# Kernel optimization log

Hardware: AMD Instinct MI355X
Metric: run time of the kernel (lower is better)

## Reference

```python
import jax, jax.numpy as jnp
import numpy as np

N, E, D, C, H = 50000, 800000, 128, 64, 2
NEG_SLOPE = 0.2


def gat_layer(x, src, dst, W, a_src, a_dst, b, heads, concat):
    # PyG GATConv (eval mode: attention dropout disabled), add_self_loops already in src/dst.
    n = x.shape[0]
    c = W.shape[1] // heads
    xl = (x @ W).reshape(n, heads, c)                      # [N,H,C]
    s = jnp.einsum('nhc,hc->nh', xl, a_src)                # alpha_src per node
    d = jnp.einsum('nhc,hc->nh', xl, a_dst)                # alpha_dst per node
    e = jax.nn.leaky_relu(s[src] + d[dst], NEG_SLOPE)      # [E,H]
    emax = jax.lax.stop_gradient(jax.ops.segment_max(e, dst, num_segments=n))
    ex = jnp.exp(e - emax[dst])
    denom = jax.ops.segment_sum(ex, dst, num_segments=n)   # every node has a self-loop -> denom > 0
    alpha = ex / denom[dst]                                # softmax over incoming edges
    msg = xl[src] * alpha[:, :, None]                      # [E,H,C]
    out = jax.ops.segment_sum(msg, dst, num_segments=n)    # [N,H,C]
    out = out.reshape(n, heads * c) if concat else out.mean(axis=1)
    return out + b


def setup_inputs() -> dict:
    key = jax.random.key(0)
    ks = jax.random.split(key, 16)
    x = jax.random.normal(ks[0], (N, D), dtype=jnp.float32)
    edge_index = jax.random.randint(ks[1], (2, E), 0, N, dtype=jnp.int64)
    def glorot(k, shape):
        fan = shape[0] + shape[-1]
        return jax.random.normal(k, shape, dtype=jnp.float32) * np.sqrt(2.0 / fan).astype(np.float32)
    # layer 0: D -> H*C (concat)
    W0 = glorot(ks[2], (D, H * C)); att_src0 = glorot(ks[3], (H, C)); att_dst0 = glorot(ks[4], (H, C)); b0 = jnp.zeros((H * C,), jnp.float32)
    # layer 1: H*C -> H*C (concat)
    W1 = glorot(ks[5], (H * C, H * C)); att_src1 = glorot(ks[6], (H, C)); att_dst1 = glorot(ks[7], (H, C)); b1 = jnp.zeros((H * C,), jnp.float32)
    # layer 2: H*C -> C (heads=1, concat=False)
    W2 = glorot(ks[8], (H * C, C)); att_src2 = glorot(ks[9], (1, C)); att_dst2 = glorot(ks[10], (1, C)); b2 = jnp.zeros((C,), jnp.float32)
    return dict(x=x, edge_index=edge_index,
                W0=W0, att_src0=att_src0, att_dst0=att_dst0, b0=b0,
                W1=W1, att_src1=att_src1, att_dst1=att_dst1, b1=b1,
                W2=W2, att_src2=att_src2, att_dst2=att_dst2, b2=b2)


def reference(x, edge_index, W0, att_src0, att_dst0, b0, W1, att_src1, att_dst1, b1, W2, att_src2, att_dst2, b2):
    n = x.shape[0]
    loops = jnp.arange(n, dtype=edge_index.dtype)
    src = jnp.concatenate([edge_index[0], loops])
    dst = jnp.concatenate([edge_index[1], loops])
    h = gat_layer(x, src, dst, W0, att_src0, att_dst0, b0, H, True)
    h = jax.nn.elu(h)
    h = gat_layer(h, src, dst, W1, att_src1, att_dst1, b1, H, True)
    h = jax.nn.elu(h)
    h = gat_layer(h, src, dst, W2, att_src2, att_dst2, b2, 1, False)
    return h
```

## Files before the change

### kernel.cpp

```cpp
#include <hip/hip_runtime.h>
#include <hip/hip_fp16.h>
#include <math.h>

#define NEG_SLOPE 0.2f
#define RSTRIDE_LOG 6
#define RSTRIDE (1 << RSTRIDE_LOG)

__device__ __forceinline__ float lrelu(float v) { return v > 0.0f ? v : NEG_SLOPE * v; }

typedef _Float16 half8 __attribute__((ext_vector_type(8)));
typedef float floatx4 __attribute__((ext_vector_type(4)));


__global__ __launch_bounds__(256) void cvt_wt3_init_k(const float* __restrict__ W0,
                                                      const float* __restrict__ W1,
                                                      const float* __restrict__ W2,
                                                      __half* __restrict__ Wt0,
                                                      __half* __restrict__ Wt1,
                                                      __half* __restrict__ Wt2,
                                                      int* __restrict__ cursor, int n) {
  const int i = blockIdx.x * 256 + threadIdx.x;
  const int stride = gridDim.x * 256;
  for (int k = i; k < n; k += stride) cursor[k] = k << RSTRIDE_LOG;
  if (i < 128 * 128) {
    int col = i >> 7, k = i & 127;
    Wt0[i] = __float2half(W0[k * 128 + col]);
    Wt1[i] = __float2half(W1[k * 128 + col]);
    if (col < 64) Wt2[(size_t)col * 128 + k] = __float2half(W2[k * 64 + col]);
  }
}


__global__ __launch_bounds__(256) void scatter_win_k(const int* __restrict__ src,
                                                     const int* __restrict__ dst,
                                                     int* __restrict__ cursor,
                                                     int* __restrict__ csr,
                                                     int e, int winSize) {
  const int win = blockIdx.x & 7;
  const int lo = win * winSize;
  const int hi = lo + winSize;
  const int base = (blockIdx.x >> 3) * 4096 + threadIdx.x;
  for (int t = 0; t < 16; ++t) {
    int i = base + t * 256;
    if (i < e) {
      int d = dst[i];
      if (d >= lo && d < hi) {
        int pos = atomicAdd(&cursor[d], 1);
        if (pos < ((d + 1) << RSTRIDE_LOG)) csr[pos] = src[i];
      }
    }
  }
}


template<int M, int H_, bool IN_F32>
__global__ __launch_bounds__(256) void gemm_attn_mfma_k(const void* __restrict__ Xin,
                                                        const __half* __restrict__ Wt,
                                                        const float* __restrict__ a_src,
                                                        const float* __restrict__ a_dst,
                                                        __half* __restrict__ Yh,
                                                        float* __restrict__ sArr,
                                                        float* __restrict__ dArr, int n) {
  constexpr int CT = M / 16;
  constexpr int LP = 136;
  __shared__ _Float16 Xs[64 * LP];
  __shared__ _Float16 Ws[M * LP];
  const int tid = threadIdx.x;
  const int w = tid >> 6;
  const int lane = tid & 63;
  const int l15 = lane & 15;
  const int quad = lane >> 4;
  const int rb = blockIdx.x * 64;

  if (IN_F32) {
    const float* Xf = (const float*)Xin;
    for (int t = 0; t < 8; ++t) {
      int idx = tid + t * 256;
      int r = idx >> 5, c4 = idx & 31;
      float4 v = make_float4(0.f, 0.f, 0.f, 0.f);
      if (rb + r < n) v = *(const float4*)(Xf + (size_t)(rb + r) * 128 + c4 * 4);
      __half2 a = __floats2half2_rn(v.x, v.y);
      __half2 b = __floats2half2_rn(v.z, v.w);
      uint2 pk;
      pk.x = *(unsigned int*)&a;
      pk.y = *(unsigned int*)&b;
      *(uint2*)&Xs[r * LP + c4 * 4] = pk;
    }
  } else {
    const __half* Xh = (const __half*)Xin;
    for (int t = 0; t < 4; ++t) {
      int idx = tid + t * 256;
      int r = idx >> 4, c8 = idx & 15;
      uint4 v = make_uint4(0, 0, 0, 0);
      if (rb + r < n) v = *(const uint4*)(Xh + (size_t)(rb + r) * 128 + c8 * 8);
      *(uint4*)&Xs[r * LP + c8 * 8] = v;
    }
  }
  for (int t = 0; t < CT; ++t) {
    int idx = tid + t * 256;
    int r = idx >> 4, c8 = idx & 15;
    *(uint4*)&Ws[r * LP + c8 * 8] = *(const uint4*)(Wt + (size_t)r * 128 + c8 * 8);
  }
  __syncthreads();

  floatx4 acc[CT];
  for (int c = 0; c < CT; ++c)
    for (int j = 0; j < 4; ++j) acc[c][j] = 0.f;

  const int arow = w * 16 + l15;
  for (int kq = 0; kq < 4; ++kq) {
    half8 a = *(const half8*)&Xs[arow * LP + kq * 32 + quad * 8];
    for (int c = 0; c < CT; ++c) {
      half8 b = *(const half8*)&Ws[(c * 16 + l15) * LP + kq * 32 + quad * 8];
      acc[c] = __builtin_amdgcn_mfma_f32_16x16x32_f16(a, b, acc[c], 0, 0, 0);
    }
  }

  float as[CT], ad[CT];
  for (int c = 0; c < CT; ++c) {
    as[c] = a_src[c * 16 + l15];
    ad[c] = a_dst[c * 16 + l15];
  }

  for (int c = 0; c < CT; ++c) {
    for (int r = 0; r < 4; ++r) {
      int row = rb + w * 16 + quad * 4 + r;
      if (row < n) Yh[(size_t)row * M + c * 16 + l15] = __float2half(acc[c][r]);
    }
  }

  for (int r = 0; r < 4; ++r) {
    int row = rb + w * 16 + quad * 4 + r;
    float s0 = 0.f, d0 = 0.f, s1 = 0.f, d1 = 0.f;
    if (H_ == 2) {
      for (int c = 0; c < CT / 2; ++c) {
        s0 += acc[c][r] * as[c];
        d0 += acc[c][r] * ad[c];
      }
      for (int c = CT / 2; c < CT; ++c) {
        s1 += acc[c][r] * as[c];
        d1 += acc[c][r] * ad[c];
      }
    } else {
      for (int c = 0; c < CT; ++c) {
        s0 += acc[c][r] * as[c];
        d0 += acc[c][r] * ad[c];
      }
    }
    for (int o = 1; o < 16; o <<= 1) {
      s0 += __shfl_xor(s0, o);
      d0 += __shfl_xor(d0, o);
      if (H_ == 2) {
        s1 += __shfl_xor(s1, o);
        d1 += __shfl_xor(d1, o);
      }
    }
    if (l15 == 0 && row < n) {
      if (H_ == 2) {
        sArr[row * 2] = s0;
        sArr[row * 2 + 1] = s1;
        dArr[row * 2] = d0;
        dArr[row * 2 + 1] = d1;
      } else {
        sArr[row] = s0;
        dArr[row] = d0;
      }
    }
  }
}


__global__ __launch_bounds__(256) void edge2h_k(const __half* __restrict__ xlh,
                                                const float* __restrict__ sArr,
                                                const float* __restrict__ dArr,
                                                const float* __restrict__ bias,
                                                const int* __restrict__ cursor,
                                                const int* __restrict__ csr,
                                                __half* __restrict__ outh, int n) {
  const int tid = threadIdx.x;
  const int wid = tid >> 6;
  const int lane = tid & 63;
  const int sub = lane >> 4;
  const int l16 = lane & 15;
  const int nodeBase = blockIdx.x * 16;

  __shared__ int curS[16];
  __shared__ int idxS[16 * RSTRIDE];
  if (tid < 16) {
    int nn = nodeBase + tid;
    curS[tid] = (nn < n) ? cursor[nn] : 0;
  }
  __syncthreads();
  for (int t = tid; t < 16 * RSTRIDE; t += 256) {
    int li2 = t >> RSTRIDE_LOG, j = t & (RSTRIDE - 1);
    int node2 = nodeBase + li2;
    if (node2 < n) {
      int dg = curS[li2] - (node2 << RSTRIDE_LOG);
      if (j < dg) idxS[t] = csr[(node2 << RSTRIDE_LOG) + j];
    }
  }
  __syncthreads();

  const int li = (wid << 2) + sub;
  const int node = nodeBase + li;
  if (node >= n) return;
  int deg = curS[li] - (node << RSTRIDE_LOG);
  if (deg > RSTRIDE) deg = RSTRIDE;
  const int head = l16 >> 3;
  const uint4* __restrict__ xq = (const uint4*)xlh;
  const float dnsel = dArr[node * 2 + head];

  float svS = sArr[node * 2 + head];
  uint4 pS = xq[(size_t)node * 16 + l16];

  float a0 = 0.f, a1 = 0.f, a2 = 0.f, a3 = 0.f;
  float a4 = 0.f, a5 = 0.f, a6 = 0.f, a7 = 0.f;
  float den = 0.f;

  const int* __restrict__ ip = &idxS[li << RSTRIDE_LOG];
  int j = 0;
  for (; j + 4 <= deg; j += 4) {
    int idx[4];
    float sv[4];
    uint4 p[4];
#pragma unroll
    for (int t = 0; t < 4; ++t) idx[t] = ip[j + t];
#pragma unroll
    for (int t = 0; t < 4; ++t) sv[t] = sArr[idx[t] * 2 + head];
#pragma unroll
    for (int t = 0; t < 4; ++t) p[t] = xq[(size_t)idx[t] * 16 + l16];
#pragma unroll
    for (int t = 0; t < 4; ++t) {
      float w = __expf(lrelu(sv[t] + dnsel));
      den += w;
      float2 v0 = __half22float2(*(__half2*)&p[t].x);
      float2 v1 = __half22float2(*(__half2*)&p[t].y);
      float2 v2 = __half22float2(*(__half2*)&p[t].z);
      float2 v3 = __half22float2(*(__half2*)&p[t].w);
      a0 += w * v0.x; a1 += w * v0.y; a2 += w * v1.x; a3 += w * v1.y;
      a4 += w * v2.x; a5 += w * v2.y; a6 += w * v3.x; a7 += w * v3.y;
    }
  }
  for (; j < deg; ++j) {
    int i0 = ip[j];
    float sv = sArr[i0 * 2 + head];
    uint4 p = xq[(size_t)i0 * 16 + l16];
    float w = __expf(lrelu(sv + dnsel));
    den += w;
    float2 v0 = __half22float2(*(__half2*)&p.x);
    float2 v1 = __half22float2(*(__half2*)&p.y);
    float2 v2 = __half22float2(*(__half2*)&p.z);
    float2 v3 = __half22float2(*(__half2*)&p.w);
    a0 += w * v0.x; a1 += w * v0.y; a2 += w * v1.x; a3 += w * v1.y;
    a4 += w * v2.x; a5 += w * v2.y; a6 += w * v3.x; a7 += w * v3.y;
  }

  float wS = __expf(lrelu(svS + dnsel));
  den += wS;
  {
    float2 v0 = __half22float2(*(__half2*)&pS.x);
    float2 v1 = __half22float2(*(__half2*)&pS.y);
    float2 v2 = __half22float2(*(__half2*)&pS.z);
    float2 v3 = __half22float2(*(__half2*)&pS.w);
    a0 += wS * v0.x; a1 += wS * v0.y; a2 += wS * v1.x; a3 += wS * v1.y;
    a4 += wS * v2.x; a5 += wS * v2.y; a6 += wS * v3.x; a7 += wS * v3.y;
  }

  float wi = 1.f / den;
  float4 bbA = ((const float4*)bias)[l16 * 2];
  float4 bbB = ((const float4*)bias)[l16 * 2 + 1];
  float r0 = a0 * wi + bbA.x;
  float r1 = a1 * wi + bbA.y;
  float r2 = a2 * wi + bbA.z;
  float r3 = a3 * wi + bbA.w;
  float r4 = a4 * wi + bbB.x;
  float r5 = a5 * wi + bbB.y;
  float r6 = a6 * wi + bbB.z;
  float r7 = a7 * wi + bbB.w;
  r0 = r0 > 0.f ? r0 : expm1f(r0);
  r1 = r1 > 0.f ? r1 : expm1f(r1);
  r2 = r2 > 0.f ? r2 : expm1f(r2);
  r3 = r3 > 0.f ? r3 : expm1f(r3);
  r4 = r4 > 0.f ? r4 : expm1f(r4);
  r5 = r5 > 0.f ? r5 : expm1f(r5);
  r6 = r6 > 0.f ? r6 : expm1f(r6);
  r7 = r7 > 0.f ? r7 : expm1f(r7);
  __half2 h0 = __floats2half2_rn(r0, r1);
  __half2 h1 = __floats2half2_rn(r2, r3);
  __half2 h2 = __floats2half2_rn(r4, r5);
  __half2 h3 = __floats2half2_rn(r6, r7);
  uint4 pk;
  pk.x = *(unsigned int*)&h0;
  pk.y = *(unsigned int*)&h1;
  pk.z = *(unsigned int*)&h2;
  pk.w = *(unsigned int*)&h3;
  ((uint4*)outh)[(size_t)node * 16 + l16] = pk;
}

__global__ __launch_bounds__(256) void edge1h_k(const __half* __restrict__ xlh,
                                                const float* __restrict__ sArr,
                                                const float* __restrict__ dArr,
                                                const float* __restrict__ bias,
                                                const int* __restrict__ cursor,
                                                const int* __restrict__ csr,
                                                float* __restrict__ outp, int n) {
  const int tid = threadIdx.x;
  const int wid = tid >> 6;
  const int lane = tid & 63;
  const int sub = lane >> 4;
  const int l16 = lane & 15;
  const int nodeBase = blockIdx.x * 16;

  __shared__ int curS[16];
  __shared__ int idxS[16 * RSTRIDE];
  if (tid < 16) {
    int nn = nodeBase + tid;
    curS[tid] = (nn < n) ? cursor[nn] : 0;
  }
  __syncthreads();
  for (int t = tid; t < 16 * RSTRIDE; t += 256) {
    int li2 = t >> RSTRIDE_LOG, j = t & (RSTRIDE - 1);
    int node2 = nodeBase + li2;
    if (node2 < n) {
      int dg = curS[li2] - (node2 << RSTRIDE_LOG);
      if (j < dg) idxS[t] = csr[(node2 << RSTRIDE_LOG) + j];
    }
  }
  __syncthreads();

  const int li = (wid << 2) + sub;
  const int node = nodeBase + li;
  if (node >= n) return;
  int deg = curS[li] - (node << RSTRIDE_LOG);
  if (deg > RSTRIDE) deg = RSTRIDE;
  const uint2* __restrict__ xq = (const uint2*)xlh;
  const float dn = dArr[node];

  float svS = sArr[node];
  uint2 pS = xq[(size_t)node * 16 + l16];

  float a0 = 0.f, a1 = 0.f, a2 = 0.f, a3 = 0.f;
  float den = 0.f;

  const int* __restrict__ ip = &idxS[li << RSTRIDE_LOG];
  int j = 0;
  for (; j + 4 <= deg; j += 4) {
    int idx[4];
    float sv[4];
    uint2 p[4];
#pragma unroll
    for (int t = 0; t < 4; ++t) idx[t] = ip[j + t];
#pragma unroll
    for (int t = 0; t < 4; ++t) sv[t] = sArr[idx[t]];
#pragma unroll
    for (int t = 0; t < 4; ++t) p[t] = xq[(size_t)idx[t] * 16 + l16];
#pragma unroll
    for (int t = 0; t < 4; ++t) {
      float w = __expf(lrelu(sv[t] + dn));
      den += w;
      float2 v0 = __half22float2(*(__half2*)&p[t].x);
      float2 v1 = __half22float2(*(__half2*)&p[t].y);
      a0 += w * v0.x; a1 += w * v0.y; a2 += w * v1.x; a3 += w * v1.y;
    }
  }
  for (; j < deg; ++j) {
    int i0 = ip[j];
    float sv = sArr[i0];
    uint2 p = xq[(size_t)i0 * 16 + l16];
    float w = __expf(lrelu(sv + dn));
    den += w;
    float2 v0 = __half22float2(*(__half2*)&p.x);
    float2 v1 = __half22float2(*(__half2*)&p.y);
    a0 += w * v0.x; a1 += w * v0.y; a2 += w * v1.x; a3 += w * v1.y;
  }

  float wS = __expf(lrelu(svS + dn));
  den += wS;
  {
    float2 v0 = __half22float2(*(__half2*)&pS.x);
    float2 v1 = __half22float2(*(__half2*)&pS.y);
    a0 += wS * v0.x; a1 += wS * v0.y; a2 += wS * v1.x; a3 += wS * v1.y;
  }

  float wi = 1.f / den;
  float4 bb = ((const float4*)bias)[l16];
  float4 r;
  r.x = a0 * wi + bb.x;
  r.y = a1 * wi + bb.y;
  r.z = a2 * wi + bb.z;
  r.w = a3 * wi + bb.w;
  ((float4*)outp)[(size_t)node * 16 + l16] = r;
}


extern "C" void kernel_launch(void* const* d_in, const int* in_sizes, int n_in,
                              void* d_out, int out_size, void* d_ws, size_t ws_size,
                              hipStream_t stream) {
  const float* x  = (const float*)d_in[0];
  const int* ei   = (const int*)d_in[1];
  const float* W0 = (const float*)d_in[2];
  const float* as0 = (const float*)d_in[3];
  const float* ad0 = (const float*)d_in[4];
  const float* b0 = (const float*)d_in[5];
  const float* W1 = (const float*)d_in[6];
  const float* as1 = (const float*)d_in[7];
  const float* ad1 = (const float*)d_in[8];
  const float* b1 = (const float*)d_in[9];
  const float* W2 = (const float*)d_in[10];
  const float* as2 = (const float*)d_in[11];
  const float* ad2 = (const float*)d_in[12];
  const float* b2 = (const float*)d_in[13];
  float* out = (float*)d_out;

  const int n = in_sizes[0] / 128;
  const int e = in_sizes[1] / 2;
  const int* srcIdx = ei;
  const int* dstIdx = ei + e;

  float* ws = (float*)d_ws;
  float* sArr = ws;
  float* dArr = sArr + (size_t)n * 2;
  __half* xlh = (__half*)(dArr + (size_t)n * 2);
  __half* bufHh = xlh + (size_t)n * 128;
  __half* Wt0 = bufHh + (size_t)n * 128;
  __half* Wt1 = Wt0 + 128 * 128;
  __half* Wt2 = Wt1 + 128 * 128;
  int* csr = (int*)(Wt2 + 64 * 128);
  int* cursor = csr + (size_t)n * RSTRIDE;

  const int nb = (n + 255) / 256;
  const int winSize = (n + 7) / 8;
  const int gwin = 8 * ((e + 4095) / 4096);

  cvt_wt3_init_k<<<nb, 256, 0, stream>>>(W0, W1, W2, Wt0, Wt1, Wt2, cursor, n);
  scatter_win_k<<<gwin, 256, 0, stream>>>(srcIdx, dstIdx, cursor, csr, e, winSize);

  const int gb = (n + 63) / 64;
  const int gq = (n + 15) / 16;

  gemm_attn_mfma_k<128, 2, true><<<gb, 256, 0, stream>>>(x, Wt0, as0, ad0, xlh, sArr, dArr, n);
  edge2h_k<<<gq, 256, 0, stream>>>(xlh, sArr, dArr, b0, cursor, csr, bufHh, n);

  gemm_attn_mfma_k<128, 2, false><<<gb, 256, 0, stream>>>(bufHh, Wt1, as1, ad1, xlh, sArr, dArr, n);
  edge2h_k<<<gq, 256, 0, stream>>>(xlh, sArr, dArr, b1, cursor, csr, bufHh, n);

  gemm_attn_mfma_k<64, 1, false><<<gb, 256, 0, stream>>>(bufHh, Wt2, as2, ad2, xlh, sArr, dArr, n);
  edge1h_k<<<gq, 256, 0, stream>>>(xlh, sArr, dArr, b2, cursor, csr, out, n);
}
```

Measured before the change: 260.4 us.

## Fuse CSR scatter into first GEMM launch to overlap independent work

```diff
diff --git a/kernel.cpp b/kernel.cpp
--- a/kernel.cpp
+++ b/kernel.cpp
@@ -31,46 +31,23 @@
 }
 
 
-__global__ __launch_bounds__(256) void scatter_win_k(const int* __restrict__ src,
-                                                     const int* __restrict__ dst,
-                                                     int* __restrict__ cursor,
-                                                     int* __restrict__ csr,
-                                                     int e, int winSize) {
-  const int win = blockIdx.x & 7;
-  const int lo = win * winSize;
-  const int hi = lo + winSize;
-  const int base = (blockIdx.x >> 3) * 4096 + threadIdx.x;
-  for (int t = 0; t < 16; ++t) {
-    int i = base + t * 256;
-    if (i < e) {
-      int d = dst[i];
-      if (d >= lo && d < hi) {
-        int pos = atomicAdd(&cursor[d], 1);
-        if (pos < ((d + 1) << RSTRIDE_LOG)) csr[pos] = src[i];
-      }
-    }
-  }
-}
-
-
 template<int M, int H_, bool IN_F32>
-__global__ __launch_bounds__(256) void gemm_attn_mfma_k(const void* __restrict__ Xin,
-                                                        const __half* __restrict__ Wt,
-                                                        const float* __restrict__ a_src,
-                                                        const float* __restrict__ a_dst,
-                                                        __half* __restrict__ Yh,
-                                                        float* __restrict__ sArr,
-                                                        float* __restrict__ dArr, int n) {
+__device__ __forceinline__ void gemm_body(_Float16* Xs, _Float16* Ws,
+                                          const void* __restrict__ Xin,
+                                          const __half* __restrict__ Wt,
+                                          const float* __restrict__ a_src,
+                                          const float* __restrict__ a_dst,
+                                          __half* __restrict__ Yh,
+                                          float* __restrict__ sArr,
+                                          float* __restrict__ dArr, int n, int tile) {
   constexpr int CT = M / 16;
   constexpr int LP = 136;
-  __shared__ _Float16 Xs[64 * LP];
-  __shared__ _Float16 Ws[M * LP];
   const int tid = threadIdx.x;
   const int w = tid >> 6;
   const int lane = tid & 63;
   const int l15 = lane & 15;
   const int quad = lane >> 4;
-  const int rb = blockIdx.x * 64;
+  const int rb = tile * 64;
 
   if (IN_F32) {
     const float* Xf = (const float*)Xin;
@@ -164,6 +141,56 @@
       } else {
         sArr[row] = s0;
         dArr[row] = d0;
+      }
+    }
+  }
+}
+
+
+template<int M, int H_, bool IN_F32>
+__global__ __launch_bounds__(256) void gemm_attn_mfma_k(const void* __restrict__ Xin,
+                                                        const __half* __restrict__ Wt,
+                                                        const float* __restrict__ a_src,
+                                                        const float* __restrict__ a_dst,
+                                                        __half* __restrict__ Yh,
+                                                        float* __restrict__ sArr,
+                                                        float* __restrict__ dArr, int n) {
+  __shared__ _Float16 Xs[64 * 136];
+  __shared__ _Float16 Ws[M * 136];
+  gemm_body<M, H_, IN_F32>(Xs, Ws, Xin, Wt, a_src, a_dst, Yh, sArr, dArr, n, blockIdx.x);
+}
+
+
+__global__ __launch_bounds__(256) void gemm0_scatter_k(const void* __restrict__ Xin,
+                                                       const __half* __restrict__ Wt0,
+                                                       const float* __restrict__ a_src,
+                                                       const float* __restrict__ a_dst,
+                                                       __half* __restrict__ Yh,
+                                                       float* __restrict__ sArr,
+                                                       float* __restrict__ dArr, int n, int gb,
+                                                       const int* __restrict__ src,
+                                                       const int* __restrict__ dst,
+                                                       int* __restrict__ cursor,
+                                                       int* __restrict__ csr,
+                                                       int e, int winSize) {
+  __shared__ _Float16 Xs[64 * 136];
+  __shared__ _Float16 Ws[128 * 136];
+  if ((int)blockIdx.x < gb) {
+    gemm_body<128, 2, true>(Xs, Ws, Xin, Wt0, a_src, a_dst, Yh, sArr, dArr, n, blockIdx.x);
+  } else {
+    const int vb = blockIdx.x - gb;
+    const int win = vb & 7;
+    const int lo = win * winSize;
+    const int hi = lo + winSize;
+    const int base = (vb >> 3) * 4096 + threadIdx.x;
+    for (int t = 0; t < 16; ++t) {
+      int i = base + t * 256;
+      if (i < e) {
+        int d = dst[i];
+        if (d >= lo && d < hi) {
+          int pos = atomicAdd(&cursor[d], 1);
+          if (pos < ((d + 1) << RSTRIDE_LOG)) csr[pos] = src[i];
+        }
       }
     }
   }
@@ -431,14 +458,13 @@
   const int nb = (n + 255) / 256;
   const int winSize = (n + 7) / 8;
   const int gwin = 8 * ((e + 4095) / 4096);
-
-  cvt_wt3_init_k<<<nb, 256, 0, stream>>>(W0, W1, W2, Wt0, Wt1, Wt2, cursor, n);
-  scatter_win_k<<<gwin, 256, 0, stream>>>(srcIdx, dstIdx, cursor, csr, e, winSize);
-
   const int gb = (n + 63) / 64;
   const int gq = (n + 15) / 16;
 
-  gemm_attn_mfma_k<128, 2, true><<<gb, 256, 0, stream>>>(x, Wt0, as0, ad0, xlh, sArr, dArr, n);
+  cvt_wt3_init_k<<<nb, 256, 0, stream>>>(W0, W1, W2, Wt0, Wt1, Wt2, cursor, n);
+
+  gemm0_scatter_k<<<gb + gwin, 256, 0, stream>>>(x, Wt0, as0, ad0, xlh, sArr, dArr, n, gb,
+                                                 srcIdx, dstIdx, cursor, csr, e, winSize);
   edge2h_k<<<gq, 256, 0, stream>>>(xlh, sArr, dArr, b0, cursor, csr, bufHh, n);
 
   gemm_attn_mfma_k<128, 2, false><<<gb, 256, 0, stream>>>(bufHh, Wt1, as1, ad1, xlh, sArr, dArr, n);
```

Result: no change. 265.5 us (+2.0%).

## Merge CSR scatter into layer-0 GEMM launch as extra blocks

Applied to the files above, without the earlier changes.

```diff
diff --git a/kernel.cpp b/kernel.cpp
--- a/kernel.cpp
+++ b/kernel.cpp
@@ -31,23 +31,111 @@
 }
 
 
-__global__ __launch_bounds__(256) void scatter_win_k(const int* __restrict__ src,
-                                                     const int* __restrict__ dst,
-                                                     int* __restrict__ cursor,
-                                                     int* __restrict__ csr,
-                                                     int e, int winSize) {
-  const int win = blockIdx.x & 7;
-  const int lo = win * winSize;
-  const int hi = lo + winSize;
-  const int base = (blockIdx.x >> 3) * 4096 + threadIdx.x;
-  for (int t = 0; t < 16; ++t) {
-    int i = base + t * 256;
-    if (i < e) {
-      int d = dst[i];
-      if (d >= lo && d < hi) {
-        int pos = atomicAdd(&cursor[d], 1);
-        if (pos < ((d + 1) << RSTRIDE_LOG)) csr[pos] = src[i];
+__global__ __launch_bounds__(256) void gemm0_scatter_k(const float* __restrict__ Xf,
+                                                       const __half* __restrict__ Wt,
+                                                       const float* __restrict__ a_src,
+                                                       const float* __restrict__ a_dst,
+                                                       __half* __restrict__ Yh,
+                                                       float* __restrict__ sArr,
+                                                       float* __restrict__ dArr, int n, int gb,
+                                                       const int* __restrict__ src,
+                                                       const int* __restrict__ dst,
+                                                       int* __restrict__ cursor,
+                                                       int* __restrict__ csr,
+                                                       int e, int winSize) {
+  constexpr int CT = 8;
+  constexpr int LP = 136;
+  __shared__ _Float16 Xs[64 * LP];
+  const int tid = threadIdx.x;
+
+  if ((int)blockIdx.x >= gb) {
+    const int vb = blockIdx.x - gb;
+    const int win = vb & 7;
+    const int lo = win * winSize;
+    const int hi = lo + winSize;
+    const int base = (vb >> 3) * 4096 + tid;
+    for (int t = 0; t < 16; ++t) {
+      int i = base + t * 256;
+      if (i < e) {
+        int d = dst[i];
+        if (d >= lo && d < hi) {
+          int pos = atomicAdd(&cursor[d], 1);
+          if (pos < ((d + 1) << RSTRIDE_LOG)) csr[pos] = src[i];
+        }
       }
+    }
+    return;
+  }
+
+  const int w = tid >> 6;
+  const int lane = tid & 63;
+  const int l15 = lane & 15;
+  const int quad = lane >> 4;
+  const int rb = blockIdx.x * 64;
+
+  for (int t = 0; t < 8; ++t) {
+    int idx = tid + t * 256;
+    int r = idx >> 5, c4 = idx & 31;
+    float4 v = make_float4(0.f, 0.f, 0.f, 0.f);
+    if (rb + r < n) v = *(const float4*)(Xf + (size_t)(rb + r) * 128 + c4 * 4);
+    __half2 a = __floats2half2_rn(v.x, v.y);
+    __half2 b = __floats2half2_rn(v.z, v.w);
+    uint2 pk;
+    pk.x = *(unsigned int*)&a;
+    pk.y = *(unsigned int*)&b;
+    *(uint2*)&Xs[r * LP + c4 * 4] = pk;
+  }
+  __syncthreads();
+
+  floatx4 acc[CT];
+  for (int c = 0; c < CT; ++c)
+    for (int j = 0; j < 4; ++j) acc[c][j] = 0.f;
+
+  const int arow = w * 16 + l15;
+  const _Float16* __restrict__ Wg = (const _Float16*)Wt;
+  for (int kq = 0; kq < 4; ++kq) {
+    half8 a = *(const half8*)&Xs[arow * LP + kq * 32 + quad * 8];
+    for (int c = 0; c < CT; ++c) {
+      half8 b = *(const half8*)&Wg[(size_t)(c * 16 + l15) * 128 + kq * 32 + quad * 8];
+      acc[c] = __builtin_amdgcn_mfma_f32_16x16x32_f16(a, b, acc[c], 0, 0, 0);
+    }
+  }
+
+  float as[CT], ad[CT];
+  for (int c = 0; c < CT; ++c) {
+    as[c] = a_src[c * 16 + l15];
+    ad[c] = a_dst[c * 16 + l15];
+  }
+
+  for (int c = 0; c < CT; ++c) {
+    for (int r = 0; r < 4; ++r) {
+      int row = rb + w * 16 + quad * 4 + r;
+      if (row < n) Yh[(size_t)row * 128 + c * 16 + l15] = __float2half(acc[c][r]);
+    }
+  }
+
+  for (int r = 0; r < 4; ++r) {
+    int row = rb + w * 16 + quad * 4 + r;
+    float s0 = 0.f, d0 = 0.f, s1 = 0.f, d1 = 0.f;
+    for (int c = 0; c < CT / 2; ++c) {
+      s0 += acc[c][r] * as[c];
+      d0 += acc[c][r] * ad[c];
+    }
+    for (int c = CT / 2; c < CT; ++c) {
+      s1 += acc[c][r] * as[c];
+      d1 += acc[c][r] * ad[c];
+    }
+    for (int o = 1; o < 16; o <<= 1) {
+      s0 += __shfl_xor(s0, o);
+      d0 += __shfl_xor(d0, o);
+      s1 += __shfl_xor(s1, o);
+      d1 += __shfl_xor(d1, o);
+    }
+    if (l15 == 0 && row < n) {
+      sArr[row * 2] = s0;
+      sArr[row * 2 + 1] = s1;
+      dArr[row * 2] = d0;
+      dArr[row * 2 + 1] = d1;
     }
   }
 }
@@ -431,14 +519,13 @@
   const int nb = (n + 255) / 256;
   const int winSize = (n + 7) / 8;
   const int gwin = 8 * ((e + 4095) / 4096);
-
-  cvt_wt3_init_k<<<nb, 256, 0, stream>>>(W0, W1, W2, Wt0, Wt1, Wt2, cursor, n);
-  scatter_win_k<<<gwin, 256, 0, stream>>>(srcIdx, dstIdx, cursor, csr, e, winSize);
-
   const int gb = (n + 63) / 64;
   const int gq = (n + 15) / 16;
 
-  gemm_attn_mfma_k<128, 2, true><<<gb, 256, 0, stream>>>(x, Wt0, as0, ad0, xlh, sArr, dArr, n);
+  cvt_wt3_init_k<<<nb, 256, 0, stream>>>(W0, W1, W2, Wt0, Wt1, Wt2, cursor, n);
+
+  gemm0_scatter_k<<<gb + gwin, 256, 0, stream>>>(x, Wt0, as0, ad0, xlh, sArr, dArr, n, gb,
+                                                 srcIdx, dstIdx, cursor, csr, e, winSize);
   edge2h_k<<<gq, 256, 0, stream>>>(xlh, sArr, dArr, b0, cursor, csr, bufHh, n);
 
   gemm_attn_mfma_k<128, 2, false><<<gb, 256, 0, stream>>>(bufHh, Wt1, as1, ad1, xlh, sArr, dArr, n);
```

Measured after the change: 265.9 us. 2.1% more time.

## Split each node's edges across four 16-lane subgroups per wavefront

Applied to the files above, without the earlier changes.

```diff
diff --git a/kernel.cpp b/kernel.cpp
--- a/kernel.cpp
+++ b/kernel.cpp
@@ -182,69 +182,39 @@
   const int lane = tid & 63;
   const int sub = lane >> 4;
   const int l16 = lane & 15;
-  const int nodeBase = blockIdx.x * 16;
-
-  __shared__ int curS[16];
-  __shared__ int idxS[16 * RSTRIDE];
-  if (tid < 16) {
+  const int nodeBase = blockIdx.x * 4;
+  const int node = nodeBase + wid;
+
+  __shared__ int curS[4];
+  __shared__ int idxS[4 * RSTRIDE];
+  if (tid < 4) {
     int nn = nodeBase + tid;
     curS[tid] = (nn < n) ? cursor[nn] : 0;
   }
   __syncthreads();
-  for (int t = tid; t < 16 * RSTRIDE; t += 256) {
-    int li2 = t >> RSTRIDE_LOG, j = t & (RSTRIDE - 1);
+  {
+    int li2 = tid >> RSTRIDE_LOG, j = tid & (RSTRIDE - 1);
     int node2 = nodeBase + li2;
     if (node2 < n) {
       int dg = curS[li2] - (node2 << RSTRIDE_LOG);
-      if (j < dg) idxS[t] = csr[(node2 << RSTRIDE_LOG) + j];
+      if (j < dg) idxS[tid] = csr[(node2 << RSTRIDE_LOG) + j];
     }
   }
   __syncthreads();
 
-  const int li = (wid << 2) + sub;
-  const int node = nodeBase + li;
   if (node >= n) return;
-  int deg = curS[li] - (node << RSTRIDE_LOG);
+  int deg = curS[wid] - (node << RSTRIDE_LOG);
   if (deg > RSTRIDE) deg = RSTRIDE;
   const int head = l16 >> 3;
   const uint4* __restrict__ xq = (const uint4*)xlh;
   const float dnsel = dArr[node * 2 + head];
 
-  float svS = sArr[node * 2 + head];
-  uint4 pS = xq[(size_t)node * 16 + l16];
-
   float a0 = 0.f, a1 = 0.f, a2 = 0.f, a3 = 0.f;
   float a4 = 0.f, a5 = 0.f, a6 = 0.f, a7 = 0.f;
   float den = 0.f;
-
-  const int* __restrict__ ip = &idxS[li << RSTRIDE_LOG];
-  int j = 0;
-  for (; j + 4 <= deg; j += 4) {
-    int idx[4];
-    float sv[4];
-    uint4 p[4];
-#pragma unroll
-    for (int t = 0; t < 4; ++t) idx[t] = ip[j + t];
-#pragma unroll
-    for (int t = 0; t < 4; ++t) sv[t] = sArr[idx[t] * 2 + head];
-#pragma unroll
-    for (int t = 0; t < 4; ++t) p[t] = xq[(size_t)idx[t] * 16 + l16];
-#pragma unroll
-    for (int t = 0; t < 4; ++t) {
-      float w = __expf(lrelu(sv[t] + dnsel));
-      den += w;
-      float2 v0 = __half22float2(*(__half2*)&p[t].x);
-      float2 v1 = __half22float2(*(__half2*)&p[t].y);
-      float2 v2 = __half22float2(*(__half2*)&p[t].z);
-      float2 v3 = __half22float2(*(__half2*)&p[t].w);
-      a0 += w * v0.x; a1 += w * v0.y; a2 += w * v1.x; a3 += w * v1.y;
-      a4 += w * v2.x; a5 += w * v2.y; a6 += w * v3.x; a7 += w * v3.y;
-    }
-  }
-  for (; j < deg; ++j) {
-    int i0 = ip[j];
-    float sv = sArr[i0 * 2 + head];
-    uint4 p = xq[(size_t)i0 * 16 + l16];
+  const int* __restrict__ ip = &idxS[wid << RSTRIDE_LOG];
+
+  auto edge_acc = [&](float sv, const uint4& p) {
     float w = __expf(lrelu(sv + dnsel));
     den += w;
     float2 v0 = __half22float2(*(__half2*)&p.x);
@@ -253,18 +223,43 @@
     float2 v3 = __half22float2(*(__half2*)&p.w);
     a0 += w * v0.x; a1 += w * v0.y; a2 += w * v1.x; a3 += w * v1.y;
     a4 += w * v2.x; a5 += w * v2.y; a6 += w * v3.x; a7 += w * v3.y;
-  }
-
-  float wS = __expf(lrelu(svS + dnsel));
-  den += wS;
-  {
-    float2 v0 = __half22float2(*(__half2*)&pS.x);
-    float2 v1 = __half22float2(*(__half2*)&pS.y);
-    float2 v2 = __half22float2(*(__half2*)&pS.z);
-    float2 v3 = __half22float2(*(__half2*)&pS.w);
-    a0 += wS * v0.x; a1 += wS * v0.y; a2 += wS * v1.x; a3 += wS * v1.y;
-    a4 += wS * v2.x; a5 += wS * v2.y; a6 += wS * v3.x; a7 += wS * v3.y;
-  }
+  };
+
+  if (sub == 0) {
+    float svS = sArr[node * 2 + head];
+    uint4 pS = xq[(size_t)node * 16 + l16];
+    edge_acc(svS, pS);
+  }
+
+  int j = sub;
+  for (; j + 12 < deg; j += 16) {
+    int idx[4];
+    float sv[4];
+    uint4 p[4];
+#pragma unroll
+    for (int t = 0; t < 4; ++t) idx[t] = ip[j + t * 4];
+#pragma unroll
+    for (int t = 0; t < 4; ++t) sv[t] = sArr[idx[t] * 2 + head];
+#pragma unroll
+    for (int t = 0; t < 4; ++t) p[t] = xq[(size_t)idx[t] * 16 + l16];
+#pragma unroll
+    for (int t = 0; t < 4; ++t) edge_acc(sv[t], p[t]);
+  }
+  for (; j < deg; j += 4) {
+    int i0 = ip[j];
+    float sv = sArr[i0 * 2 + head];
+    uint4 p = xq[(size_t)i0 * 16 + l16];
+    edge_acc(sv, p);
+  }
+
+  for (int o = 16; o <= 32; o <<= 1) {
+    a0 += __shfl_xor(a0, o); a1 += __shfl_xor(a1, o);
+    a2 += __shfl_xor(a2, o); a3 += __shfl_xor(a3, o);
+    a4 += __shfl_xor(a4, o); a5 += __shfl_xor(a5, o);
+    a6 += __shfl_xor(a6, o); a7 += __shfl_xor(a7, o);
+    den += __shfl_xor(den, o);
+  }
+  if (sub != 0) return;
 
   float wi = 1.f / den;
   float4 bbA = ((const float4*)bias)[l16 * 2];
@@ -309,78 +304,77 @@
   const int lane = tid & 63;
   const int sub = lane >> 4;
   const int l16 = lane & 15;
-  const int nodeBase = blockIdx.x * 16;
-
-  __shared__ int curS[16];
-  __shared__ int idxS[16 * RSTRIDE];
-  if (tid < 16) {
+  const int nodeBase = blockIdx.x * 4;
+  const int node = nodeBase + wid;
+
+  __shared__ int curS[4];
+  __shared__ int idxS[4 * RSTRIDE];
+  if (tid < 4) {
     int nn = nodeBase + tid;
     curS[tid] = (nn < n) ? cursor[nn] : 0;
   }
   __syncthreads();
-  for (int t = tid; t < 16 * RSTRIDE; t += 256) {
-    int li2 = t >> RSTRIDE_LOG, j = t & (RSTRIDE - 1);
+  {
+    int li2 = tid >> RSTRIDE_LOG, j = tid & (RSTRIDE - 1);
     int node2 = nodeBase + li2;
     if (node2 < n) {
       int dg = curS[li2] - (node2 << RSTRIDE_LOG);
-      if (j < dg) idxS[t] = csr[(node2 << RSTRIDE_LOG) + j];
+      if (j < dg) idxS[tid] = csr[(node2 << RSTRIDE_LOG) + j];
     }
   }
   __syncthreads();
 
-  const int li = (wid << 2) + sub;
-  const int node = nodeBase + li;
   if (node >= n) return;
-  int deg = curS[li] - (node << RSTRIDE_LOG);
+  int deg = curS[wid] - (node << RSTRIDE_LOG);
   if (deg > RSTRIDE) deg = RSTRIDE;
   const uint2* __restrict__ xq = (const uint2*)xlh;
   const float dn = dArr[node];
 
-  float svS = sArr[node];
-  uint2 pS = xq[(size_t)node * 16 + l16];
-
   float a0 = 0.f, a1 = 0.f, a2 = 0.f, a3 = 0.f;
   float den = 0.f;
-
-  const int* __restrict__ ip = &idxS[li << RSTRIDE_LOG];
-  int j = 0;
-  for (; j + 4 <= deg; j += 4) {
-    int idx[4];
-    float sv[4];
-    uint2 p[4];
-#pragma unroll
-    for (int t = 0; t < 4; ++t) idx[t] = ip[j + t];
-#pragma unroll
-    for (int t = 0; t < 4; ++t) sv[t] = sArr[idx[t]];
-#pragma unroll
-    for (int t = 0; t < 4; ++t) p[t] = xq[(size_t)idx[t] * 16 + l16];
-#pragma unroll
-    for (int t = 0; t < 4; ++t) {
-      float w = __expf(lrelu(sv[t] + dn));
-      den += w;
-      float2 v0 = __half22float2(*(__half2*)&p[t].x);
-      float2 v1 = __half22float2(*(__half2*)&p[t].y);
-      a0 += w * v0.x; a1 += w * v0.y; a2 += w * v1.x; a3 += w * v1.y;
-    }
-  }
-  for (; j < deg; ++j) {
-    int i0 = ip[j];
-    float sv = sArr[i0];
-    uint2 p = xq[(size_t)i0 * 16 + l16];
+  const int* __restrict__ ip = &idxS[wid << RSTRIDE_LOG];
+
+  auto edge_acc = [&](float sv, const uint2& p) {
     float w = __expf(lrelu(sv + dn));
     den += w;
     float2 v0 = __half22float2(*(__half2*)&p.x);
     float2 v1 = __half22float2(*(__half2*)&p.y);
     a0 += w * v0.x; a1 += w * v0.y; a2 += w * v1.x; a3 += w * v1.y;
-  }
-
-  float wS = __expf(lrelu(svS + dn));
-  den += wS;
-  {
-    float2 v0 = __half22float2(*(__half2*)&pS.x);
-    float2 v1 = __half22float2(*(__half2*)&pS.y);
-    a0 += wS * v0.x; a1 += wS * v0.y; a2 += wS * v1.x; a3 += wS * v1.y;
-  }
+  };
+
+  if (sub == 0) {
+    float svS = sArr[node];
+    uint2 pS = xq[(size_t)node * 16 + l16];
+    edge_acc(svS, pS);
+  }
+
+  int j = sub;
+  for (; j + 12 < deg; j += 16) {
+    int idx[4];
+    float sv[4];
+    uint2 p[4];
+#pragma unroll
+    for (int t = 0; t < 4; ++t) idx[t] = ip[j + t * 4];
+#pragma unroll
+    for (int t = 0; t < 4; ++t) sv[t] = sArr[idx[t]];
+#pragma unroll
+    for (int t = 0; t < 4; ++t) p[t] = xq[(size_t)idx[t] * 16 + l16];
+#pragma unroll
+    for (int t = 0; t < 4; ++t) edge_acc(sv[t], p[t]);
+  }
+  for (; j < deg; j += 4) {
+    int i0 = ip[j];
+    float sv = sArr[i0];
+    uint2 p = xq[(size_t)i0 * 16 + l16];
+    edge_acc(sv, p);
+  }
+
+  for (int o = 16; o <= 32; o <<= 1) {
+    a0 += __shfl_xor(a0, o); a1 += __shfl_xor(a1, o);
+    a2 += __shfl_xor(a2, o); a3 += __shfl_xor(a3, o);
+    den += __shfl_xor(den, o);
+  }
+  if (sub != 0) return;
 
   float wi = 1.f / den;
   float4 bb = ((const float4*)bias)[l16];
@@ -431,13 +425,12 @@
   const int nb = (n + 255) / 256;
   const int winSize = (n + 7) / 8;
   const int gwin = 8 * ((e + 4095) / 4096);
+  const int gb = (n + 63) / 64;
+  const int gq = (n + 3) / 4;
 
   cvt_wt3_init_k<<<nb, 256, 0, stream>>>(W0, W1, W2, Wt0, Wt1, Wt2, cursor, n);
   scatter_win_k<<<gwin, 256, 0, stream>>>(srcIdx, dstIdx, cursor, csr, e, winSize);
 
-  const int gb = (n + 63) / 64;
-  const int gq = (n + 15) / 16;
-
   gemm_attn_mfma_k<128, 2, true><<<gb, 256, 0, stream>>>(x, Wt0, as0, ad0, xlh, sArr, dArr, n);
   edge2h_k<<<gq, 256, 0, stream>>>(xlh, sArr, dArr, b0, cursor, csr, bufHh, n);
 
```

Result: slower. 279.7 us (+7.4%).
